# Performance work log

Measured on AMD Instinct MI355X. Metric: run time of the kernel, lower is better.

Reference implementation:

```python
import jax, jax.numpy as jnp
import numpy as np
from math import sqrt

N_HEAD = 8

def setup_inputs() -> dict:
    key = jax.random.key(0)
    ks = jax.random.split(key, 9)
    B, L, D = 4, 2048, 512
    s = 0.02
    return {
        "queries": jax.random.normal(ks[0], (B, L, D), jnp.float32),
        "keys": jax.random.normal(ks[1], (B, L, D), jnp.float32),
        "values": jax.random.normal(ks[2], (B, L, D), jnp.float32),
        "Wq": jax.random.normal(ks[3], (D, D), jnp.float32) * s,
        "bq": jax.random.normal(ks[4], (D,), jnp.float32) * s,
        "Wk": jax.random.normal(ks[5], (D, D), jnp.float32) * s,
        "bk": jax.random.normal(ks[6], (D,), jnp.float32) * s,
        "Wv": jax.random.normal(ks[7], (D, D), jnp.float32) * s,
        "bv": jax.random.normal(ks[8], (D,), jnp.float32) * s,
    }

def reference(queries, keys, values, Wq, bq, Wk, bk, Wv, bv):
    B, L, D = queries.shape
    H = N_HEAD
    E = D // H  # head dim
    # q/k/v linear projections, split into heads: [B, L, H, E]
    q = (queries @ Wq + bq).reshape(B, L, H, E)
    k = (keys @ Wk + bk).reshape(B, -1, H, E)
    v = (values @ Wv + bv).reshape(B, -1, H, E)
    # scores: [B, H, L, L_k]; source applies scale AFTER matmul, mask=False path
    scores = jnp.einsum("blhe,bmhe->bhlm", q, k)
    scale = 1.0 / sqrt(E)
    attn = jax.nn.softmax(scores * scale, axis=-1)  # [B, H, L, L_k]
    out = jnp.einsum("bhlm,bmhe->blhe", attn, v)    # [B, L, H, E]
    out = out.reshape(B, L, H * E)
    return (out, attn)
```

## Files before the change

kernel.cpp:

```cpp
#include <hip/hip_runtime.h>
#include <hip/hip_bf16.h>
#include <stdint.h>

typedef __bf16 bf16x8 __attribute__((ext_vector_type(8)));
typedef float f32x4 __attribute__((ext_vector_type(4)));
typedef unsigned short u16x8 __attribute__((ext_vector_type(8)));

#define SCALE_LOG2E 0.18033688011112042f

__device__ __forceinline__ unsigned short f2bf(float f) {
    union { float f; unsigned u; } v; v.f = f;
    unsigned r = v.u + 0x7FFFu + ((v.u >> 16) & 1u);
    return (unsigned short)(r >> 16);
}

__device__ __forceinline__ bf16x8 ld_frag(const unsigned short* p) {
    u16x8 u = *(const u16x8*)p;
    return __builtin_bit_cast(bf16x8, u);
}

__global__ void wt_kernel(const float* __restrict__ W, unsigned short* __restrict__ Wt) {
    int idx = blockIdx.x * blockDim.x + threadIdx.x;
    int k = idx >> 9, n = idx & 511;
    Wt[n * 512 + k] = f2bf(W[idx]);
}

__global__ __launch_bounds__(256)
void proj_kernel(const float* __restrict__ X, const unsigned short* __restrict__ Wt,
                 const float* __restrict__ bias, unsigned short* __restrict__ Out) {
    __shared__ unsigned short Xs[64 * 64];
    __shared__ unsigned short Ws[64 * 64];
    const int tid = threadIdx.x;
    const int wave = tid >> 6, lane = tid & 63;
    const int quad = lane >> 4, l16 = lane & 15;
    const int m0 = blockIdx.x * 64;
    const int n0 = blockIdx.y * 64;

    f32x4 acc[4] = {};

    for (int kc = 0; kc < 512; kc += 64) {
        #pragma unroll
        for (int i = 0; i < 4; i++) {
            int e = tid + i * 256;
            int row = e >> 4;
            int c4 = (e & 15) * 4;
            const float4 v = *(const float4*)&X[(size_t)(m0 + row) * 512 + kc + c4];
            unsigned short* d = &Xs[row * 64 + c4];
            d[0] = f2bf(v.x); d[1] = f2bf(v.y); d[2] = f2bf(v.z); d[3] = f2bf(v.w);
        }
        #pragma unroll
        for (int i = 0; i < 2; i++) {
            int e = tid + i * 256;
            int row = e >> 3;
            int c8 = (e & 7) * 8;
            *(u16x8*)&Ws[row * 64 + c8] = *(const u16x8*)&Wt[(size_t)(n0 + row) * 512 + kc + c8];
        }
        __syncthreads();
        #pragma unroll
        for (int ks = 0; ks < 2; ks++) {
            bf16x8 a = ld_frag(&Xs[(wave * 16 + l16) * 64 + ks * 32 + quad * 8]);
            #pragma unroll
            for (int nn = 0; nn < 4; nn++) {
                bf16x8 b = ld_frag(&Ws[(nn * 16 + l16) * 64 + ks * 32 + quad * 8]);
                acc[nn] = __builtin_amdgcn_mfma_f32_16x16x32_bf16(a, b, acc[nn], 0, 0, 0);
            }
        }
        __syncthreads();
    }
    #pragma unroll
    for (int nn = 0; nn < 4; nn++) {
        int n = n0 + nn * 16 + l16;
        float bv = bias[n];
        #pragma unroll
        for (int r = 0; r < 4; r++) {
            int m = m0 + wave * 16 + quad * 4 + r;
            Out[(size_t)m * 512 + n] = f2bf(acc[nn][r] + bv);
        }
    }
}

__global__ __launch_bounds__(256)
void attn_kernel(const unsigned short* __restrict__ qb,
                 const unsigned short* __restrict__ kb,
                 const unsigned short* __restrict__ vb,
                 float* __restrict__ out, float* __restrict__ attn) {
    __shared__ unsigned short Qs[64 * 64];
    __shared__ unsigned short Ks[64 * 64];
    __shared__ unsigned short Vt[64 * 64];
    __shared__ unsigned short Ps[64 * 64];

    const int tid = threadIdx.x;
    const int wave = tid >> 6, lane = tid & 63;
    const int quad = lane >> 4, l16 = lane & 15;
    const int mt = blockIdx.x;
    const int h  = blockIdx.y;
    const int b  = blockIdx.z;
    const int m0 = mt * 64;

    const unsigned short* Qg = qb + (size_t)b * 2048 * 512 + h * 64;
    const unsigned short* Kg = kb + (size_t)b * 2048 * 512 + h * 64;
    const unsigned short* Vg = vb + (size_t)b * 2048 * 512 + h * 64;

    #pragma unroll
    for (int i = 0; i < 2; i++) {
        int e = tid + i * 256;
        int row = e >> 3;
        int c8 = (e & 7) * 8;
        *(u16x8*)&Qs[row * 64 + c8] = *(const u16x8*)&Qg[(size_t)(m0 + row) * 512 + c8];
    }
    __syncthreads();

    f32x4 o[4] = {};
    float lsum[4] = {0.f, 0.f, 0.f, 0.f};

    for (int t = 0; t < 32; t++) {
        const int j0 = t * 64;
        #pragma unroll
        for (int i = 0; i < 2; i++) {
            int e = tid + i * 256;
            int row = e >> 3;
            int c8 = (e & 7) * 8;
            *(u16x8*)&Ks[row * 64 + c8] = *(const u16x8*)&Kg[(size_t)(j0 + row) * 512 + c8];
        }
        #pragma unroll
        for (int i = 0; i < 2; i++) {
            int e = tid + i * 256;
            int row = e >> 3;
            int c8 = (e & 7) * 8;
            u16x8 v = *(const u16x8*)&Vg[(size_t)(j0 + row) * 512 + c8];
            #pragma unroll
            for (int q2 = 0; q2 < 8; q2++) Vt[(c8 + q2) * 64 + row] = v[q2];
        }
        __syncthreads();
        f32x4 s[4] = {};
        #pragma unroll
        for (int ks = 0; ks < 2; ks++) {
            bf16x8 a = ld_frag(&Qs[(wave * 16 + l16) * 64 + ks * 32 + quad * 8]);
            #pragma unroll
            for (int nn = 0; nn < 4; nn++) {
                bf16x8 bf = ld_frag(&Ks[(nn * 16 + l16) * 64 + ks * 32 + quad * 8]);
                s[nn] = __builtin_amdgcn_mfma_f32_16x16x32_bf16(a, bf, s[nn], 0, 0, 0);
            }
        }
        #pragma unroll
        for (int nn = 0; nn < 4; nn++) {
            #pragma unroll
            for (int r = 0; r < 4; r++) {
                float p = exp2f(s[nn][r] * SCALE_LOG2E);
                lsum[r] += p;
                Ps[(wave * 16 + quad * 4 + r) * 64 + nn * 16 + l16] = f2bf(p);
            }
        }
        __syncthreads();
        #pragma unroll
        for (int ks = 0; ks < 2; ks++) {
            bf16x8 a = ld_frag(&Ps[(wave * 16 + l16) * 64 + ks * 32 + quad * 8]);
            #pragma unroll
            for (int nn = 0; nn < 4; nn++) {
                bf16x8 bf = ld_frag(&Vt[(nn * 16 + l16) * 64 + ks * 32 + quad * 8]);
                o[nn] = __builtin_amdgcn_mfma_f32_16x16x32_bf16(a, bf, o[nn], 0, 0, 0);
            }
        }
        __syncthreads();
    }

    #pragma unroll
    for (int r = 0; r < 4; r++) {
        float v = lsum[r];
        v += __shfl_xor(v, 1);
        v += __shfl_xor(v, 2);
        v += __shfl_xor(v, 4);
        v += __shfl_xor(v, 8);
        lsum[r] = v;
    }
    float inv[4];
    #pragma unroll
    for (int r = 0; r < 4; r++) inv[r] = 1.0f / lsum[r];

    float* og = out + (size_t)b * 2048 * 512 + h * 64;
    #pragma unroll
    for (int nn = 0; nn < 4; nn++) {
        #pragma unroll
        for (int r = 0; r < 4; r++) {
            int m = m0 + wave * 16 + quad * 4 + r;
            og[(size_t)m * 512 + nn * 16 + l16] = o[nn][r] * inv[r];
        }
    }

    float* ag = attn + ((size_t)(b * 8 + h)) * 2048 * 2048;
    for (int t = 0; t < 32; t++) {
        const int j0 = t * 64;
        __syncthreads();
        #pragma unroll
        for (int i = 0; i < 2; i++) {
            int e = tid + i * 256;
            int row = e >> 3;
            int c8 = (e & 7) * 8;
            *(u16x8*)&Ks[row * 64 + c8] = *(const u16x8*)&Kg[(size_t)(j0 + row) * 512 + c8];
        }
        __syncthreads();
        f32x4 s[4] = {};
        #pragma unroll
        for (int ks = 0; ks < 2; ks++) {
            bf16x8 a = ld_frag(&Qs[(wave * 16 + l16) * 64 + ks * 32 + quad * 8]);
            #pragma unroll
            for (int nn = 0; nn < 4; nn++) {
                bf16x8 bf = ld_frag(&Ks[(nn * 16 + l16) * 64 + ks * 32 + quad * 8]);
                s[nn] = __builtin_amdgcn_mfma_f32_16x16x32_bf16(a, bf, s[nn], 0, 0, 0);
            }
        }
        #pragma unroll
        for (int nn = 0; nn < 4; nn++) {
            #pragma unroll
            for (int r = 0; r < 4; r++) {
                int m = m0 + wave * 16 + quad * 4 + r;
                float p = exp2f(s[nn][r] * SCALE_LOG2E) * inv[r];
                ag[(size_t)m * 2048 + j0 + nn * 16 + l16] = p;
            }
        }
    }
}

extern "C" void kernel_launch(void* const* d_in, const int* in_sizes, int n_in,
                              void* d_out, int out_size, void* d_ws, size_t ws_size,
                              hipStream_t stream) {
    const float* queries = (const float*)d_in[0];
    const float* keys    = (const float*)d_in[1];
    const float* values  = (const float*)d_in[2];
    const float* Wq = (const float*)d_in[3];
    const float* bq = (const float*)d_in[4];
    const float* Wk = (const float*)d_in[5];
    const float* bk = (const float*)d_in[6];
    const float* Wv = (const float*)d_in[7];
    const float* bv = (const float*)d_in[8];

    float* out  = (float*)d_out;
    float* attn = out + (size_t)4 * 2048 * 512;

    unsigned short* ws  = (unsigned short*)d_ws;
    unsigned short* Wtq = ws;
    unsigned short* Wtk = Wtq + 512 * 512;
    unsigned short* Wtv = Wtk + 512 * 512;
    unsigned short* qb  = Wtv + 512 * 512;
    unsigned short* kb  = qb + (size_t)8192 * 512;
    unsigned short* vb  = kb + (size_t)8192 * 512;

    dim3 bt(256);
    wt_kernel<<<dim3(512 * 512 / 256), bt, 0, stream>>>(Wq, Wtq);
    wt_kernel<<<dim3(512 * 512 / 256), bt, 0, stream>>>(Wk, Wtk);
    wt_kernel<<<dim3(512 * 512 / 256), bt, 0, stream>>>(Wv, Wtv);

    proj_kernel<<<dim3(128, 8), bt, 0, stream>>>(queries, Wtq, bq, qb);
    proj_kernel<<<dim3(128, 8), bt, 0, stream>>>(keys,    Wtk, bk, kb);
    proj_kernel<<<dim3(128, 8), bt, 0, stream>>>(values,  Wtv, bv, vb);

    attn_kernel<<<dim3(32, 8, 4), bt, 0, stream>>>(qb, kb, vb, out, attn);
}
```

Baseline: 852.4 us.

## Swizzle LDS tiles, pre-transpose V in projection, keep Q fragments in registers

Applies an XOR swizzle to all 64x64 LDS tiles so row-strided MFMA fragment reads avoid bank conflicts. The V projection now writes a head-major transposed layout, so the attention kernel loads V^T with vector copies instead of doing a scalar scatter-transpose into LDS. Q fragments are loaded once into registers and reused for every key tile. The kernel stays dominated by the fp32 attention-matrix writes, so the overall gain may be limited.

```diff
diff --git a/kernel.cpp b/kernel.cpp
--- a/kernel.cpp
+++ b/kernel.cpp
@@ -5,6 +5,7 @@
 typedef __bf16 bf16x8 __attribute__((ext_vector_type(8)));
 typedef float f32x4 __attribute__((ext_vector_type(4)));
 typedef unsigned short u16x8 __attribute__((ext_vector_type(8)));
+typedef unsigned short u16x4 __attribute__((ext_vector_type(4)));
 
 #define SCALE_LOG2E 0.18033688011112042f
 
@@ -19,12 +20,17 @@
     return __builtin_bit_cast(bf16x8, u);
 }
 
+__device__ __forceinline__ int swz(int row, int col) {
+    return (row * 64 + col) ^ ((row & 7) << 3);
+}
+
 __global__ void wt_kernel(const float* __restrict__ W, unsigned short* __restrict__ Wt) {
     int idx = blockIdx.x * blockDim.x + threadIdx.x;
     int k = idx >> 9, n = idx & 511;
     Wt[n * 512 + k] = f2bf(W[idx]);
 }
 
+template <int TRANS>
 __global__ __launch_bounds__(256)
 void proj_kernel(const float* __restrict__ X, const unsigned short* __restrict__ Wt,
                  const float* __restrict__ bias, unsigned short* __restrict__ Out) {
@@ -45,36 +51,52 @@
             int row = e >> 4;
             int c4 = (e & 15) * 4;
             const float4 v = *(const float4*)&X[(size_t)(m0 + row) * 512 + kc + c4];
-            unsigned short* d = &Xs[row * 64 + c4];
-            d[0] = f2bf(v.x); d[1] = f2bf(v.y); d[2] = f2bf(v.z); d[3] = f2bf(v.w);
-        }
-        #pragma unroll
-        for (int i = 0; i < 2; i++) {
-            int e = tid + i * 256;
-            int row = e >> 3;
-            int c8 = (e & 7) * 8;
-            *(u16x8*)&Ws[row * 64 + c8] = *(const u16x8*)&Wt[(size_t)(n0 + row) * 512 + kc + c8];
-        }
-        __syncthreads();
-        #pragma unroll
-        for (int ks = 0; ks < 2; ks++) {
-            bf16x8 a = ld_frag(&Xs[(wave * 16 + l16) * 64 + ks * 32 + quad * 8]);
-            #pragma unroll
-            for (int nn = 0; nn < 4; nn++) {
-                bf16x8 b = ld_frag(&Ws[(nn * 16 + l16) * 64 + ks * 32 + quad * 8]);
+            u16x4 pk;
+            pk[0] = f2bf(v.x); pk[1] = f2bf(v.y); pk[2] = f2bf(v.z); pk[3] = f2bf(v.w);
+            *(u16x4*)&Xs[swz(row, c4)] = pk;
+        }
+        #pragma unroll
+        for (int i = 0; i < 2; i++) {
+            int e = tid + i * 256;
+            int row = e >> 3;
+            int c8 = (e & 7) * 8;
+            *(u16x8*)&Ws[swz(row, c8)] = *(const u16x8*)&Wt[(size_t)(n0 + row) * 512 + kc + c8];
+        }
+        __syncthreads();
+        #pragma unroll
+        for (int ks = 0; ks < 2; ks++) {
+            bf16x8 a = ld_frag(&Xs[swz(wave * 16 + l16, ks * 32 + quad * 8)]);
+            #pragma unroll
+            for (int nn = 0; nn < 4; nn++) {
+                bf16x8 b = ld_frag(&Ws[swz(nn * 16 + l16, ks * 32 + quad * 8)]);
                 acc[nn] = __builtin_amdgcn_mfma_f32_16x16x32_bf16(a, b, acc[nn], 0, 0, 0);
             }
         }
         __syncthreads();
     }
-    #pragma unroll
-    for (int nn = 0; nn < 4; nn++) {
-        int n = n0 + nn * 16 + l16;
-        float bv = bias[n];
-        #pragma unroll
-        for (int r = 0; r < 4; r++) {
-            int m = m0 + wave * 16 + quad * 4 + r;
-            Out[(size_t)m * 512 + n] = f2bf(acc[nn][r] + bv);
+    if (TRANS == 0) {
+        #pragma unroll
+        for (int nn = 0; nn < 4; nn++) {
+            int n = n0 + nn * 16 + l16;
+            float bv = bias[n];
+            #pragma unroll
+            for (int r = 0; r < 4; r++) {
+                int m = m0 + wave * 16 + quad * 4 + r;
+                Out[(size_t)m * 512 + n] = f2bf(acc[nn][r] + bv);
+            }
+        }
+    } else {
+        const int bb = m0 >> 11;
+        const int l0 = (m0 & 2047) + wave * 16 + quad * 4;
+        #pragma unroll
+        for (int nn = 0; nn < 4; nn++) {
+            int n = n0 + nn * 16 + l16;
+            float bv = bias[n];
+            int hh = n >> 6, ee = n & 63;
+            u16x4 pk;
+            #pragma unroll
+            for (int r = 0; r < 4; r++) pk[r] = f2bf(acc[nn][r] + bv);
+            *(u16x4*)&Out[((size_t)(bb * 8 + hh) * 64 + ee) * 2048 + l0] = pk;
         }
     }
 }
@@ -82,7 +104,7 @@
 __global__ __launch_bounds__(256)
 void attn_kernel(const unsigned short* __restrict__ qb,
                  const unsigned short* __restrict__ kb,
-                 const unsigned short* __restrict__ vb,
+                 const unsigned short* __restrict__ vtb,
                  float* __restrict__ out, float* __restrict__ attn) {
     __shared__ unsigned short Qs[64 * 64];
     __shared__ unsigned short Ks[64 * 64];
@@ -99,16 +121,21 @@
 
     const unsigned short* Qg = qb + (size_t)b * 2048 * 512 + h * 64;
     const unsigned short* Kg = kb + (size_t)b * 2048 * 512 + h * 64;
-    const unsigned short* Vg = vb + (size_t)b * 2048 * 512 + h * 64;
+    const unsigned short* Vg = vtb + (size_t)(b * 8 + h) * 64 * 2048;
 
     #pragma unroll
     for (int i = 0; i < 2; i++) {
         int e = tid + i * 256;
         int row = e >> 3;
         int c8 = (e & 7) * 8;
-        *(u16x8*)&Qs[row * 64 + c8] = *(const u16x8*)&Qg[(size_t)(m0 + row) * 512 + c8];
+        *(u16x8*)&Qs[swz(row, c8)] = *(const u16x8*)&Qg[(size_t)(m0 + row) * 512 + c8];
     }
     __syncthreads();
+
+    bf16x8 qf[2];
+    #pragma unroll
+    for (int ks = 0; ks < 2; ks++)
+        qf[ks] = ld_frag(&Qs[swz(wave * 16 + l16, ks * 32 + quad * 8)]);
 
     f32x4 o[4] = {};
     float lsum[4] = {0.f, 0.f, 0.f, 0.f};
@@ -120,26 +147,23 @@
             int e = tid + i * 256;
             int row = e >> 3;
             int c8 = (e & 7) * 8;
-            *(u16x8*)&Ks[row * 64 + c8] = *(const u16x8*)&Kg[(size_t)(j0 + row) * 512 + c8];
-        }
-        #pragma unroll
-        for (int i = 0; i < 2; i++) {
-            int e = tid + i * 256;
-            int row = e >> 3;
-            int c8 = (e & 7) * 8;
-            u16x8 v = *(const u16x8*)&Vg[(size_t)(j0 + row) * 512 + c8];
-            #pragma unroll
-            for (int q2 = 0; q2 < 8; q2++) Vt[(c8 + q2) * 64 + row] = v[q2];
+            *(u16x8*)&Ks[swz(row, c8)] = *(const u16x8*)&Kg[(size_t)(j0 + row) * 512 + c8];
+        }
+        #pragma unroll
+        for (int i = 0; i < 2; i++) {
+            int e = tid + i * 256;
+            int row = e >> 3;
+            int c8 = (e & 7) * 8;
+            *(u16x8*)&Vt[swz(row, c8)] = *(const u16x8*)&Vg[(size_t)row * 2048 + j0 + c8];
         }
         __syncthreads();
         f32x4 s[4] = {};
         #pragma unroll
         for (int ks = 0; ks < 2; ks++) {
-            bf16x8 a = ld_frag(&Qs[(wave * 16 + l16) * 64 + ks * 32 + quad * 8]);
-            #pragma unroll
-            for (int nn = 0; nn < 4; nn++) {
-                bf16x8 bf = ld_frag(&Ks[(nn * 16 + l16) * 64 + ks * 32 + quad * 8]);
-                s[nn] = __builtin_amdgcn_mfma_f32_16x16x32_bf16(a, bf, s[nn], 0, 0, 0);
+            #pragma unroll
+            for (int nn = 0; nn < 4; nn++) {
+                bf16x8 bf = ld_frag(&Ks[swz(nn * 16 + l16, ks * 32 + quad * 8)]);
+                s[nn] = __builtin_amdgcn_mfma_f32_16x16x32_bf16(qf[ks], bf, s[nn], 0, 0, 0);
             }
         }
         #pragma unroll
@@ -148,16 +172,16 @@
             for (int r = 0; r < 4; r++) {
                 float p = exp2f(s[nn][r] * SCALE_LOG2E);
                 lsum[r] += p;
-                Ps[(wave * 16 + quad * 4 + r) * 64 + nn * 16 + l16] = f2bf(p);
-            }
-        }
-        __syncthreads();
-        #pragma unroll
-        for (int ks = 0; ks < 2; ks++) {
-            bf16x8 a = ld_frag(&Ps[(wave * 16 + l16) * 64 + ks * 32 + quad * 8]);
-            #pragma unroll
-            for (int nn = 0; nn < 4; nn++) {
-                bf16x8 bf = ld_frag(&Vt[(nn * 16 + l16) * 64 + ks * 32 + quad * 8]);
+                Ps[swz(wave * 16 + quad * 4 + r, nn * 16 + l16)] = f2bf(p);
+            }
+        }
+        __syncthreads();
+        #pragma unroll
+        for (int ks = 0; ks < 2; ks++) {
+            bf16x8 a = ld_frag(&Ps[swz(wave * 16 + l16, ks * 32 + quad * 8)]);
+            #pragma unroll
+            for (int nn = 0; nn < 4; nn++) {
+                bf16x8 bf = ld_frag(&Vt[swz(nn * 16 + l16, ks * 32 + quad * 8)]);
                 o[nn] = __builtin_amdgcn_mfma_f32_16x16x32_bf16(a, bf, o[nn], 0, 0, 0);
             }
         }
@@ -196,17 +220,16 @@
             int e = tid + i * 256;
             int row = e >> 3;
             int c8 = (e & 7) * 8;
-            *(u16x8*)&Ks[row * 64 + c8] = *(const u16x8*)&Kg[(size_t)(j0 + row) * 512 + c8];
+            *(u16x8*)&Ks[swz(row, c8)] = *(const u16x8*)&Kg[(size_t)(j0 + row) * 512 + c8];
         }
         __syncthreads();
         f32x4 s[4] = {};
         #pragma unroll
         for (int ks = 0; ks < 2; ks++) {
-            bf16x8 a = ld_frag(&Qs[(wave * 16 + l16) * 64 + ks * 32 + quad * 8]);
-            #pragma unroll
-            for (int nn = 0; nn < 4; nn++) {
-                bf16x8 bf = ld_frag(&Ks[(nn * 16 + l16) * 64 + ks * 32 + quad * 8]);
-                s[nn] = __builtin_amdgcn_mfma_f32_16x16x32_bf16(a, bf, s[nn], 0, 0, 0);
+            #pragma unroll
+            for (int nn = 0; nn < 4; nn++) {
+                bf16x8 bf = ld_frag(&Ks[swz(nn * 16 + l16, ks * 32 + quad * 8)]);
+                s[nn] = __builtin_amdgcn_mfma_f32_16x16x32_bf16(qf[ks], bf, s[nn], 0, 0, 0);
             }
         }
         #pragma unroll
@@ -243,16 +266,16 @@
     unsigned short* Wtv = Wtk + 512 * 512;
     unsigned short* qb  = Wtv + 512 * 512;
     unsigned short* kb  = qb + (size_t)8192 * 512;
-    unsigned short* vb  = kb + (size_t)8192 * 512;
+    unsigned short* vtb = kb + (size_t)8192 * 512;
 
     dim3 bt(256);
     wt_kernel<<<dim3(512 * 512 / 256), bt, 0, stream>>>(Wq, Wtq);
     wt_kernel<<<dim3(512 * 512 / 256), bt, 0, stream>>>(Wk, Wtk);
     wt_kernel<<<dim3(512 * 512 / 256), bt, 0, stream>>>(Wv, Wtv);
 
-    proj_kernel<<<dim3(128, 8), bt, 0, stream>>>(queries, Wtq, bq, qb);
-    proj_kernel<<<dim3(128, 8), bt, 0, stream>>>(keys,    Wtk, bk, kb);
-    proj_kernel<<<dim3(128, 8), bt, 0, stream>>>(values,  Wtv, bv, vb);
-
-    attn_kernel<<<dim3(32, 8, 4), bt, 0, stream>>>(qb, kb, vb, out, attn);
-}
+    proj_kernel<0><<<dim3(128, 8), bt, 0, stream>>>(queries, Wtq, bq, qb);
+    proj_kernel<0><<<dim3(128, 8), bt, 0, stream>>>(keys,    Wtk, bk, kb);
+    proj_kernel<1><<<dim3(128, 8), bt, 0, stream>>>(values,  Wtv, bv, vtb);
+
+    attn_kernel<<<dim3(32, 8, 4), bt, 0, stream>>>(qb, kb, vtb, out, attn);
+}
```

After: 772.4 us. 1.1x faster.
